# Kernel optimization log

Hardware: AMD Instinct MI355X
Metric: run time of the kernel (lower is better)

## Reference

```python
import jax, jax.numpy as jnp
import numpy as np

N_NODES = 100000
N_EDGES = 1600000
N_GRAPHS = 512
IN_DIM = 128
D = 128
N_CLASSES = 10


def gcn_layer(x, src, dst, W, b, n_nodes):
    """PyG GCNConv: out = D^{-1/2}(A+I)D^{-1/2} (x W) + b, deg over dst col + self-loop."""
    h = x @ W  # [N, d]
    deg = jax.ops.segment_sum(jnp.ones(src.shape[0], x.dtype), dst,
                              num_segments=n_nodes) + 1.0  # self-loop adds 1
    dinv = jax.lax.rsqrt(deg)  # deg >= 1 so always finite
    norm = dinv[src] * dinv[dst]  # [E]
    agg = jax.ops.segment_sum(h[src] * norm[:, None], dst, num_segments=n_nodes)
    agg = agg + h * (dinv * dinv)[:, None]  # self-loop message: dinv_i^2 * h_i
    return agg + b


def setup_inputs() -> dict:
    key = jax.random.key(0)
    ks = jax.random.split(key, 10)
    s = 0.05
    return {
        "x": jax.random.normal(ks[0], (N_NODES, IN_DIM), jnp.float32),
        "c_2": jax.random.randint(ks[1], (N_EDGES,), 0, N_NODES, jnp.int64),
        "u_2": jax.random.randint(ks[2], (N_EDGES,), 0, N_NODES, jnp.int64),
        "batch": jnp.sort(jax.random.randint(ks[3], (N_NODES,), 0, N_GRAPHS, jnp.int64)),
        "W_enc": jax.random.normal(ks[4], (IN_DIM, D), jnp.float32) * s,
        "b_enc": jnp.zeros((D,), jnp.float32),
        "W1": jax.random.normal(ks[5], (D, D), jnp.float32) * s,
        "b1": jnp.zeros((D,), jnp.float32),
        "W2": jax.random.normal(ks[6], (D, D), jnp.float32) * s,
        "b2": jnp.zeros((D,), jnp.float32),
        "W3": jax.random.normal(ks[7], (D, D), jnp.float32) * s,
        "b3": jnp.zeros((D,), jnp.float32),
        "Wr1": jax.random.normal(ks[8], (D, D), jnp.float32) * s,
        "br1": jnp.zeros((D,), jnp.float32),
        "Wr2": jax.random.normal(ks[9], (D, N_CLASSES), jnp.float32) * s,
        "br2": jnp.zeros((N_CLASSES,), jnp.float32),
    }


def reference(x, c_2, u_2, batch, W_enc, b_enc, W1, b1, W2, b2, W3, b3,
              Wr1, br1, Wr2, br2):
    h = x @ W_enc + b_enc
    for W, b in ((W1, b1), (W2, b2), (W3, b3)):
        h = gcn_layer(h, c_2, u_2, W, b, N_NODES)
        h = jax.nn.relu(h)  # dropout is identity in eval mode
    # global_add_pool over graph assignment
    g = jax.ops.segment_sum(h, batch, num_segments=N_GRAPHS)  # [G, d]
    logits = jax.nn.relu(g @ Wr1 + br1) @ Wr2 + br2  # [G, num_classes]
    return logits
```

## Files before the change

### kernel.cpp

```cpp
#include <hip/hip_runtime.h>
#include <hip/hip_bf16.h>

#define NN 100000
#define NE 1600000
#define NG 512
#define NC 10
#define NBINS 391
#define BINCAP 5120
#define EPB 4096

typedef __attribute__((ext_vector_type(8))) short bf16x8;
typedef __attribute__((ext_vector_type(4))) float f32x4;

__device__ __forceinline__ float bflo(unsigned u) { return __uint_as_float(u << 16); }
__device__ __forceinline__ float bfhi(unsigned u) { return __uint_as_float(u & 0xffff0000u); }
__device__ __forceinline__ unsigned short f2bf(float f) {
  unsigned u = __float_as_uint(f);
  unsigned r = u + 0x7fffu + ((u >> 16) & 1u);
  return (unsigned short)(r >> 16);
}


__global__ __launch_bounds__(256) void k_binp1(const int* __restrict__ src, const int* __restrict__ dst,
                                               int* __restrict__ binCursor, unsigned* __restrict__ stage) {
  __shared__ unsigned srec[EPB];
  __shared__ unsigned short sbin[EPB];
  __shared__ int cnt[NBINS], pre[NBINS], base[NBINS], lcur[NBINS];
  __shared__ int tmp[256];
  int t = threadIdx.x;
  for (int i = t; i < NBINS; i += 256) { cnt[i] = 0; lcur[i] = 0; }
  __syncthreads();
  int e0 = blockIdx.x * EPB;
  unsigned myrec[16];
  short mybin[16];
#pragma unroll
  for (int i = 0; i < 16; ++i) {
    int e = e0 + i * 256 + t;
    if (e < NE) {
      int s = src[e], d = dst[e];
      int b = d >> 8;
      mybin[i] = (short)b;
      myrec[i] = ((unsigned)s << 8) | (unsigned)(d & 255);
      atomicAdd(&cnt[b], 1);
    } else mybin[i] = -1;
  }
  __syncthreads();
  {
    int idx0 = t * 2;
    int c0 = (idx0 < NBINS) ? cnt[idx0] : 0;
    int c1 = (idx0 + 1 < NBINS) ? cnt[idx0 + 1] : 0;
    int s = c0 + c1;
    tmp[t] = s;
    __syncthreads();
    for (int o = 1; o < 256; o <<= 1) { int v = (t >= o) ? tmp[t - o] : 0; __syncthreads(); tmp[t] += v; __syncthreads(); }
    int ex = tmp[t] - s;
    if (idx0 < NBINS) pre[idx0] = ex;
    if (idx0 + 1 < NBINS) pre[idx0 + 1] = ex + c0;
  }
  __syncthreads();
  for (int i = t; i < NBINS; i += 256) if (cnt[i] > 0) base[i] = atomicAdd(&binCursor[i], cnt[i]);
  __syncthreads();
#pragma unroll
  for (int i = 0; i < 16; ++i) {
    int b = mybin[i];
    if (b >= 0) {
      int r = atomicAdd(&lcur[b], 1);
      int pos = pre[b] + r;
      srec[pos] = myrec[i];
      sbin[pos] = (unsigned short)b;
    }
  }
  __syncthreads();
  int total = NE - e0; if (total > EPB) total = EPB;
  for (int sidx = t; sidx < total; sidx += 256) {
    int b = sbin[sidx];
    stage[base[b] + (sidx - pre[b])] = srec[sidx];
  }
}

__global__ __launch_bounds__(256) void k_binp2(const unsigned* __restrict__ stage, const int* __restrict__ binCursor,
                                               int* __restrict__ csr_src, int* __restrict__ offs,
                                               int* __restrict__ deg, float* __restrict__ dinv) {
  __shared__ int ldeg[256], loff[256], lcur[256];
  __shared__ int tmp[256];
  int b = blockIdx.x, t = threadIdx.x;
  int n0 = b << 8;
  int sbase = b * BINCAP;
  int cnt = binCursor[b] - sbase; if (cnt > BINCAP) cnt = BINCAP;
  ldeg[t] = 0;
  lcur[t] = 0;
  __syncthreads();
  for (int j = t; j < cnt; j += 256) {
    unsigned r = stage[sbase + j];
    atomicAdd(&ldeg[r & 255], 1);
  }
  __syncthreads();
  int a = ldeg[t];
  tmp[t] = a;
  __syncthreads();
  for (int o = 1; o < 256; o <<= 1) { int v = (t >= o) ? tmp[t - o] : 0; __syncthreads(); tmp[t] += v; __syncthreads(); }
  int ex = tmp[t] - a;
  loff[t] = ex;
  int node = n0 + t;
  if (node < NN) {
    offs[node] = sbase + ex;
    deg[node] = a;
    dinv[node] = rsqrtf((float)a + 1.0f);
  }
  __syncthreads();
  for (int j = t; j < cnt; j += 256) {
    unsigned r = stage[sbase + j];
    int li = r & 255;
    int pos = atomicAdd(&lcur[li], 1);
    csr_src[sbase + loff[li] + pos] = (int)(r >> 8);
  }
}

__global__ __launch_bounds__(256) void k_wt4i(const float* __restrict__ Wa, const float* __restrict__ Wb,
                                              const float* __restrict__ Wc, const float* __restrict__ Wd,
                                              unsigned short* __restrict__ Ta, unsigned short* __restrict__ Tb,
                                              unsigned short* __restrict__ Tc, unsigned short* __restrict__ Td,
                                              int* __restrict__ binCursor) {
  if (blockIdx.x == 256) {
    for (int i = threadIdx.x; i < NBINS; i += 256) binCursor[i] = i * BINCAP;
    return;
  }
  int w = blockIdx.x >> 6;
  const float* W = (w == 0) ? Wa : (w == 1) ? Wb : (w == 2) ? Wc : Wd;
  unsigned short* T = (w == 0) ? Ta : (w == 1) ? Tb : (w == 2) ? Tc : Td;
  int idx = (blockIdx.x & 63) * 256 + threadIdx.x;
  int k = idx >> 7, c = idx & 127;
  T[c * 128 + k] = f2bf(W[k * 128 + c]);
}


template<int ADD_BIAS, int RELU, int SRC_F32, int SCALE_ROW>
__global__ __launch_bounds__(256) void k_gemm_mfma(const void* __restrict__ Ap,
                                                   const unsigned short* __restrict__ Wt,
                                                   const float* __restrict__ bias,
                                                   const float* __restrict__ dinv,
                                                   unsigned short* __restrict__ Out, int M) {
  __shared__ uint4 Al4[2048];
  __shared__ uint4 Wl4[2048];
  int row0 = blockIdx.x * 128;
  const uint4* W16 = (const uint4*)Wt;
  int lane = threadIdx.x & 63;
  int wid = threadIdx.x >> 6;

  if (!SRC_F32 && row0 + 128 <= M) {
    const uint4* A16 = (const uint4*)Ap;
    int rl = lane >> 4, cc = lane & 15;
#pragma unroll
    for (int it = 0; it < 8; ++it) {
      int rbase = it * 16 + wid * 4;
      int row = rbase + rl;
      int chunk = cc ^ (row & 15);
      __builtin_amdgcn_global_load_lds(
          (const __attribute__((address_space(1))) void*)(A16 + (size_t)(row0 + row) * 16 + chunk),
          (__attribute__((address_space(3))) void*)&Al4[rbase * 16], 16, 0, 0);
      __builtin_amdgcn_global_load_lds(
          (const __attribute__((address_space(1))) void*)(W16 + (size_t)row * 16 + chunk),
          (__attribute__((address_space(3))) void*)&Wl4[rbase * 16], 16, 0, 0);
    }
  } else {
#pragma unroll
    for (int it = 0; it < 8; ++it) {
      int idx = it * 256 + threadIdx.x;
      int r = idx >> 4, c = idx & 15;
      int gr = row0 + r;
      uint4 v = make_uint4(0, 0, 0, 0);
      if (gr < M) {
        if (SRC_F32) {
          const float4* Af = (const float4*)Ap;
          float4 f0 = Af[(size_t)gr * 32 + c * 2];
          float4 f1 = Af[(size_t)gr * 32 + c * 2 + 1];
          v.x = (unsigned)f2bf(f0.x) | ((unsigned)f2bf(f0.y) << 16);
          v.y = (unsigned)f2bf(f0.z) | ((unsigned)f2bf(f0.w) << 16);
          v.z = (unsigned)f2bf(f1.x) | ((unsigned)f2bf(f1.y) << 16);
          v.w = (unsigned)f2bf(f1.z) | ((unsigned)f2bf(f1.w) << 16);
        } else {
          v = ((const uint4*)Ap)[(size_t)gr * 16 + c];
        }
      }
      Al4[r * 16 + (c ^ (r & 15))] = v;
      Wl4[r * 16 + (c ^ (r & 15))] = W16[idx];
    }
  }
  __syncthreads();

  int wr = wid >> 1, wc = wid & 1;
  int lr = lane & 15, kb = lane >> 4;

  f32x4 acc[4][4] = {};
#pragma unroll
  for (int ks = 0; ks < 4; ++ks) {
    int c = ks * 4 + kb;
    bf16x8 af[4], bfr[4];
#pragma unroll
    for (int i = 0; i < 4; ++i) {
      int ar = wr * 64 + i * 16 + lr;
      af[i] = *(const bf16x8*)&Al4[ar * 16 + (c ^ lr)];
      int bc = wc * 64 + i * 16 + lr;
      bfr[i] = *(const bf16x8*)&Wl4[bc * 16 + (c ^ lr)];
    }
#pragma unroll
    for (int i = 0; i < 4; ++i)
#pragma unroll
      for (int n = 0; n < 4; ++n)
        acc[i][n] = __builtin_amdgcn_mfma_f32_16x16x32_bf16(af[i], bfr[n], acc[i][n], 0, 0, 0);
  }

  float bcol[4];
  if (ADD_BIAS) {
#pragma unroll
    for (int n = 0; n < 4; ++n) bcol[n] = bias[wc * 64 + n * 16 + lr];
  }
#pragma unroll
  for (int i = 0; i < 4; ++i) {
    int rbase = row0 + wr * 64 + i * 16 + kb * 4;
#pragma unroll
    for (int n = 0; n < 4; ++n) {
      int col = wc * 64 + n * 16 + lr;
#pragma unroll
      for (int j = 0; j < 4; ++j) {
        int gr = rbase + j;
        if (gr < M) {
          float v = acc[i][n][j];
          if (ADD_BIAS) v += bcol[n];
          if (RELU) v = fmaxf(v, 0.f);
          if (SCALE_ROW) v *= dinv[gr];
          Out[(size_t)gr * 128 + col] = f2bf(v);
        }
      }
    }
  }
}


__global__ __launch_bounds__(256) void k_agg(const unsigned short* __restrict__ hs,
                                             const int* __restrict__ offs, const int* __restrict__ deg,
                                             const float* __restrict__ dinv,
                                             const int* __restrict__ csr_src,
                                             const float* __restrict__ bias,
                                             unsigned short* __restrict__ out) {
  int node = blockIdx.x * 4 + (threadIdx.x >> 6);
  if (node >= NN) return;
  int l = threadIdx.x & 63;
  int q = l >> 4;
  int li = l & 15;
  const uint4* hs4 = (const uint4*)hs;
  float a0 = 0.f, a1 = 0.f, a2 = 0.f, a3 = 0.f, a4 = 0.f, a5 = 0.f, a6 = 0.f, a7 = 0.f;
  if (q == 0) {
    uint4 u = hs4[(size_t)node * 16 + li];
    a0 = bflo(u.x); a1 = bfhi(u.x); a2 = bflo(u.y); a3 = bfhi(u.y);
    a4 = bflo(u.z); a5 = bfhi(u.z); a6 = bflo(u.w); a7 = bfhi(u.w);
  }
  int p0 = offs[node], n = deg[node];
  int p = 0;
  for (; p + 16 <= n; p += 16) {
    int s0 = csr_src[p0 + p + q];
    int s1 = csr_src[p0 + p + 4 + q];
    int s2 = csr_src[p0 + p + 8 + q];
    int s3 = csr_src[p0 + p + 12 + q];
    uint4 u0 = hs4[(size_t)s0 * 16 + li];
    uint4 u1 = hs4[(size_t)s1 * 16 + li];
    uint4 u2 = hs4[(size_t)s2 * 16 + li];
    uint4 u3 = hs4[(size_t)s3 * 16 + li];
    a0 += bflo(u0.x) + bflo(u1.x) + bflo(u2.x) + bflo(u3.x);
    a1 += bfhi(u0.x) + bfhi(u1.x) + bfhi(u2.x) + bfhi(u3.x);
    a2 += bflo(u0.y) + bflo(u1.y) + bflo(u2.y) + bflo(u3.y);
    a3 += bfhi(u0.y) + bfhi(u1.y) + bfhi(u2.y) + bfhi(u3.y);
    a4 += bflo(u0.z) + bflo(u1.z) + bflo(u2.z) + bflo(u3.z);
    a5 += bfhi(u0.z) + bfhi(u1.z) + bfhi(u2.z) + bfhi(u3.z);
    a6 += bflo(u0.w) + bflo(u1.w) + bflo(u2.w) + bflo(u3.w);
    a7 += bfhi(u0.w) + bfhi(u1.w) + bfhi(u2.w) + bfhi(u3.w);
  }
  for (; p + 4 <= n; p += 4) {
    int s0 = csr_src[p0 + p + q];
    uint4 u = hs4[(size_t)s0 * 16 + li];
    a0 += bflo(u.x); a1 += bfhi(u.x); a2 += bflo(u.y); a3 += bfhi(u.y);
    a4 += bflo(u.z); a5 += bfhi(u.z); a6 += bflo(u.w); a7 += bfhi(u.w);
  }
  int rem = n - p;
  if (q < rem) {
    int s0 = csr_src[p0 + p + q];
    uint4 u = hs4[(size_t)s0 * 16 + li];
    a0 += bflo(u.x); a1 += bfhi(u.x); a2 += bflo(u.y); a3 += bfhi(u.y);
    a4 += bflo(u.z); a5 += bfhi(u.z); a6 += bflo(u.w); a7 += bfhi(u.w);
  }
  a0 += __shfl_xor(a0, 16); a0 += __shfl_xor(a0, 32);
  a1 += __shfl_xor(a1, 16); a1 += __shfl_xor(a1, 32);
  a2 += __shfl_xor(a2, 16); a2 += __shfl_xor(a2, 32);
  a3 += __shfl_xor(a3, 16); a3 += __shfl_xor(a3, 32);
  a4 += __shfl_xor(a4, 16); a4 += __shfl_xor(a4, 32);
  a5 += __shfl_xor(a5, 16); a5 += __shfl_xor(a5, 32);
  a6 += __shfl_xor(a6, 16); a6 += __shfl_xor(a6, 32);
  a7 += __shfl_xor(a7, 16); a7 += __shfl_xor(a7, 32);
  if (q == 0) {
    float di = dinv[node];
    float4 b0 = ((const float4*)bias)[li * 2];
    float4 b1 = ((const float4*)bias)[li * 2 + 1];
    float r0 = fmaxf(fmaf(a0, di, b0.x), 0.f);
    float r1 = fmaxf(fmaf(a1, di, b0.y), 0.f);
    float r2 = fmaxf(fmaf(a2, di, b0.z), 0.f);
    float r3 = fmaxf(fmaf(a3, di, b0.w), 0.f);
    float r4 = fmaxf(fmaf(a4, di, b1.x), 0.f);
    float r5 = fmaxf(fmaf(a5, di, b1.y), 0.f);
    float r6 = fmaxf(fmaf(a6, di, b1.z), 0.f);
    float r7 = fmaxf(fmaf(a7, di, b1.w), 0.f);
    uint4 o;
    o.x = (unsigned)f2bf(r0) | ((unsigned)f2bf(r1) << 16);
    o.y = (unsigned)f2bf(r2) | ((unsigned)f2bf(r3) << 16);
    o.z = (unsigned)f2bf(r4) | ((unsigned)f2bf(r5) << 16);
    o.w = (unsigned)f2bf(r6) | ((unsigned)f2bf(r7) << 16);
    ((uint4*)out)[(size_t)node * 16 + li] = o;
  }
}


__device__ __forceinline__ int lowerb(const int* a, int n, int key) {
  int lo = 0, hi = n;
  while (lo < hi) {
    int mid = (lo + hi) >> 1;
    if (a[mid] < key) lo = mid + 1; else hi = mid;
  }
  return lo;
}

__global__ __launch_bounds__(256) void k_pool(const unsigned short* __restrict__ h, const int* __restrict__ batch,
                                              float* __restrict__ g) {
  __shared__ float sx[4][64];
  __shared__ float sy[4][64];
  int gi = blockIdx.x;
  int col = threadIdx.x & 63;
  int rp = threadIdx.x >> 6;
  int lo = lowerb(batch, NN, gi), hi = lowerb(batch, NN, gi + 1);
  const unsigned* h32 = (const unsigned*)h;
  float ax = 0.f, ay = 0.f;
  for (int i = lo + rp; i < hi; i += 4) {
    unsigned u = h32[(size_t)i * 64 + col];
    ax += bflo(u);
    ay += bfhi(u);
  }
  sx[rp][col] = ax;
  sy[rp][col] = ay;
  __syncthreads();
  if (rp == 0) {
    ax = sx[0][col] + sx[1][col] + sx[2][col] + sx[3][col];
    ay = sy[0][col] + sy[1][col] + sy[2][col] + sy[3][col];
    ((float2*)g)[gi * 64 + col] = make_float2(ax, ay);
  }
}

__global__ __launch_bounds__(256) void k_gemm_f32(const float* __restrict__ A, const float* __restrict__ W,
                                                  const float* __restrict__ bias, float* __restrict__ Out,
                                                  int M) {
  __shared__ float4 Wl[128 * 32];
  __shared__ float4 Xl[128 * 32];
  const float4* W4 = (const float4*)W;
  for (int i = threadIdx.x; i < 4096; i += 256) Wl[i] = W4[i];
  int row0 = blockIdx.x * 128;
  const float4* A4 = (const float4*)A;
  for (int i = threadIdx.x; i < 4096; i += 256) {
    int r = i >> 5, g = i & 31;
    int gr = row0 + r;
    float4 v = make_float4(0.f, 0.f, 0.f, 0.f);
    if (gr < M) v = A4[gr * 32 + g];
    Xl[r * 32 + (g ^ ((r >> 3) & 7))] = v;
  }
  __syncthreads();

  int cg = threadIdx.x & 15;
  int rg = threadIdx.x >> 4;
  int swz = rg & 7;
  float acc[8][8] = {};
  for (int g = 0; g < 32; ++g) {
    float4 xv[8];
#pragma unroll
    for (int i = 0; i < 8; ++i) xv[i] = Xl[(rg * 8 + i) * 32 + (g ^ swz)];
#pragma unroll
    for (int kk = 0; kk < 4; ++kk) {
      float4 wa = Wl[(g * 4 + kk) * 32 + cg * 2];
      float4 wb = Wl[(g * 4 + kk) * 32 + cg * 2 + 1];
#pragma unroll
      for (int i = 0; i < 8; ++i) {
        float x = (kk == 0) ? xv[i].x : (kk == 1) ? xv[i].y : (kk == 2) ? xv[i].z : xv[i].w;
        acc[i][0] = fmaf(x, wa.x, acc[i][0]);
        acc[i][1] = fmaf(x, wa.y, acc[i][1]);
        acc[i][2] = fmaf(x, wa.z, acc[i][2]);
        acc[i][3] = fmaf(x, wa.w, acc[i][3]);
        acc[i][4] = fmaf(x, wb.x, acc[i][4]);
        acc[i][5] = fmaf(x, wb.y, acc[i][5]);
        acc[i][6] = fmaf(x, wb.z, acc[i][6]);
        acc[i][7] = fmaf(x, wb.w, acc[i][7]);
      }
    }
  }
  float4 ba = ((const float4*)bias)[cg * 2];
  float4 bb = ((const float4*)bias)[cg * 2 + 1];
#pragma unroll
  for (int i = 0; i < 8; ++i) {
    int gr = row0 + rg * 8 + i;
    if (gr < M) {
      float4 oa, ob;
      oa.x = fmaxf(acc[i][0] + ba.x, 0.f); oa.y = fmaxf(acc[i][1] + ba.y, 0.f);
      oa.z = fmaxf(acc[i][2] + ba.z, 0.f); oa.w = fmaxf(acc[i][3] + ba.w, 0.f);
      ob.x = fmaxf(acc[i][4] + bb.x, 0.f); ob.y = fmaxf(acc[i][5] + bb.y, 0.f);
      ob.z = fmaxf(acc[i][6] + bb.z, 0.f); ob.w = fmaxf(acc[i][7] + bb.w, 0.f);
      ((float4*)Out)[gr * 32 + cg * 2] = oa;
      ((float4*)Out)[gr * 32 + cg * 2 + 1] = ob;
    }
  }
}

__global__ __launch_bounds__(128) void k_cls(const float* __restrict__ t, const float* __restrict__ Wr2,
                                             const float* __restrict__ br2, float* __restrict__ out) {
  int gi = blockIdx.x;
  __shared__ float row[128];
  row[threadIdx.x] = t[gi * 128 + threadIdx.x];
  __syncthreads();
  if (threadIdx.x < NC) {
    float acc = br2[threadIdx.x];
    for (int k = 0; k < 128; ++k) acc = fmaf(row[k], Wr2[k * NC + threadIdx.x], acc);
    out[gi * NC + threadIdx.x] = acc;
  }
}


extern "C" void kernel_launch(void* const* d_in, const int* in_sizes, int n_in,
                              void* d_out, int out_size, void* d_ws, size_t ws_size,
                              hipStream_t stream) {
  const float* x     = (const float*)d_in[0];
  const int*   src   = (const int*)d_in[1];
  const int*   dst   = (const int*)d_in[2];
  const int*   batch = (const int*)d_in[3];
  const float* W_enc = (const float*)d_in[4];
  const float* b_enc = (const float*)d_in[5];
  const float* W1 = (const float*)d_in[6],  *b1 = (const float*)d_in[7];
  const float* W2 = (const float*)d_in[8],  *b2 = (const float*)d_in[9];
  const float* W3 = (const float*)d_in[10], *b3 = (const float*)d_in[11];
  const float* Wr1 = (const float*)d_in[12], *br1 = (const float*)d_in[13];
  const float* Wr2 = (const float*)d_in[14], *br2 = (const float*)d_in[15];
  float* out = (float*)d_out;

  char* ws = (char*)d_ws;
  size_t off = 0;
  auto alloc = [&](size_t bytes) {
    void* p = ws + off;
    off = (off + bytes + 255) & ~(size_t)255;
    return p;
  };
  unsigned short* h   = (unsigned short*)alloc((size_t)NN * 128 * 2);
  unsigned short* hs  = (unsigned short*)alloc((size_t)NN * 128 * 2);
  unsigned short* WtE = (unsigned short*)alloc(128 * 128 * 2);
  unsigned short* Wt1 = (unsigned short*)alloc(128 * 128 * 2);
  unsigned short* Wt2 = (unsigned short*)alloc(128 * 128 * 2);
  unsigned short* Wt3 = (unsigned short*)alloc(128 * 128 * 2);
  int*   deg      = (int*)alloc((size_t)NN * 4);
  float* dinv     = (float*)alloc((size_t)NN * 4);
  int*   offs     = (int*)alloc((size_t)NN * 4);
  int*   binCursor= (int*)alloc(NBINS * 4);
  int*   csr_src  = (int*)alloc((size_t)NBINS * BINCAP * 4);
  unsigned* stage = (unsigned*)alloc((size_t)NBINS * BINCAP * 4);
  float* g        = (float*)alloc((size_t)NG * 128 * 4);
  float* t1       = (float*)alloc((size_t)NG * 128 * 4);

  k_wt4i<<<257, 256, 0, stream>>>(W_enc, W1, W2, W3, WtE, Wt1, Wt2, Wt3, binCursor);
  k_binp1<<<(NE + EPB - 1) / EPB, 256, 0, stream>>>(src, dst, binCursor, stage);
  k_binp2<<<NBINS, 256, 0, stream>>>(stage, binCursor, csr_src, offs, deg, dinv);

  int gM = (NN + 127) / 128;
  k_gemm_mfma<1, 0, 1, 0><<<gM, 256, 0, stream>>>(x, WtE, b_enc, nullptr, h, NN);

  const unsigned short* Wts[3] = {Wt1, Wt2, Wt3};
  const float* bs[3] = {b1, b2, b3};
  int gA = (NN + 3) / 4;
  for (int L = 0; L < 3; ++L) {
    k_gemm_mfma<0, 0, 0, 1><<<gM, 256, 0, stream>>>(h, Wts[L], nullptr, dinv, hs, NN);
    k_agg<<<gA, 256, 0, stream>>>(hs, offs, deg, dinv, csr_src, bs[L], h);
  }

  k_pool<<<NG, 256, 0, stream>>>(h, batch, g);
  k_gemm_f32<<<(NG + 127) / 128, 256, 0, stream>>>(g, Wr1, br1, t1, NG);
  k_cls<<<NG, 128, 0, stream>>>(t1, Wr2, br2, out);
}
```

Measured before the change: 399.9 us.

## Store GEMM output in feature-sliced layout and aggregate per slice

```diff
diff --git a/kernel.cpp b/kernel.cpp
--- a/kernel.cpp
+++ b/kernel.cpp
@@ -8,6 +8,7 @@
 #define NBINS 391
 #define BINCAP 5120
 #define EPB 4096
+#define NSL 8
 
 typedef __attribute__((ext_vector_type(8))) short bf16x8;
 typedef __attribute__((ext_vector_type(4))) float f32x4;
@@ -134,7 +135,7 @@
 }
 
 
-template<int ADD_BIAS, int RELU, int SRC_F32, int SCALE_ROW>
+template<int ADD_BIAS, int RELU, int SRC_F32, int SCALE_ROW, int STORE_SLICED>
 __global__ __launch_bounds__(256) void k_gemm_mfma(const void* __restrict__ Ap,
                                                    const unsigned short* __restrict__ Wt,
                                                    const float* __restrict__ bias,
@@ -229,7 +230,10 @@
           if (ADD_BIAS) v += bcol[n];
           if (RELU) v = fmaxf(v, 0.f);
           if (SCALE_ROW) v *= dinv[gr];
-          Out[(size_t)gr * 128 + col] = f2bf(v);
+          if (STORE_SLICED)
+            Out[((size_t)(col >> 4) * NN + gr) * 16 + (col & 15)] = f2bf(v);
+          else
+            Out[(size_t)gr * 128 + col] = f2bf(v);
         }
       }
     }
@@ -237,83 +241,41 @@
 }
 
 
-__global__ __launch_bounds__(256) void k_agg(const unsigned short* __restrict__ hs,
+__global__ __launch_bounds__(256) void k_agg(const unsigned short* __restrict__ hs_s,
                                              const int* __restrict__ offs, const int* __restrict__ deg,
                                              const float* __restrict__ dinv,
                                              const int* __restrict__ csr_src,
                                              const float* __restrict__ bias,
                                              unsigned short* __restrict__ out) {
-  int node = blockIdx.x * 4 + (threadIdx.x >> 6);
-  if (node >= NN) return;
-  int l = threadIdx.x & 63;
-  int q = l >> 4;
-  int li = l & 15;
-  const uint4* hs4 = (const uint4*)hs;
-  float a0 = 0.f, a1 = 0.f, a2 = 0.f, a3 = 0.f, a4 = 0.f, a5 = 0.f, a6 = 0.f, a7 = 0.f;
-  if (q == 0) {
-    uint4 u = hs4[(size_t)node * 16 + li];
-    a0 = bflo(u.x); a1 = bfhi(u.x); a2 = bflo(u.y); a3 = bfhi(u.y);
-    a4 = bflo(u.z); a5 = bfhi(u.z); a6 = bflo(u.w); a7 = bfhi(u.w);
-  }
-  int p0 = offs[node], n = deg[node];
-  int p = 0;
-  for (; p + 16 <= n; p += 16) {
-    int s0 = csr_src[p0 + p + q];
-    int s1 = csr_src[p0 + p + 4 + q];
-    int s2 = csr_src[p0 + p + 8 + q];
-    int s3 = csr_src[p0 + p + 12 + q];
-    uint4 u0 = hs4[(size_t)s0 * 16 + li];
-    uint4 u1 = hs4[(size_t)s1 * 16 + li];
-    uint4 u2 = hs4[(size_t)s2 * 16 + li];
-    uint4 u3 = hs4[(size_t)s3 * 16 + li];
-    a0 += bflo(u0.x) + bflo(u1.x) + bflo(u2.x) + bflo(u3.x);
-    a1 += bfhi(u0.x) + bfhi(u1.x) + bfhi(u2.x) + bfhi(u3.x);
-    a2 += bflo(u0.y) + bflo(u1.y) + bflo(u2.y) + bflo(u3.y);
-    a3 += bfhi(u0.y) + bfhi(u1.y) + bfhi(u2.y) + bfhi(u3.y);
-    a4 += bflo(u0.z) + bflo(u1.z) + bflo(u2.z) + bflo(u3.z);
-    a5 += bfhi(u0.z) + bfhi(u1.z) + bfhi(u2.z) + bfhi(u3.z);
-    a6 += bflo(u0.w) + bflo(u1.w) + bflo(u2.w) + bflo(u3.w);
-    a7 += bfhi(u0.w) + bfhi(u1.w) + bfhi(u2.w) + bfhi(u3.w);
-  }
-  for (; p + 4 <= n; p += 4) {
-    int s0 = csr_src[p0 + p + q];
-    uint4 u = hs4[(size_t)s0 * 16 + li];
-    a0 += bflo(u.x); a1 += bfhi(u.x); a2 += bflo(u.y); a3 += bfhi(u.y);
-    a4 += bflo(u.z); a5 += bfhi(u.z); a6 += bflo(u.w); a7 += bfhi(u.w);
-  }
-  int rem = n - p;
-  if (q < rem) {
-    int s0 = csr_src[p0 + p + q];
-    uint4 u = hs4[(size_t)s0 * 16 + li];
-    a0 += bflo(u.x); a1 += bfhi(u.x); a2 += bflo(u.y); a3 += bfhi(u.y);
-    a4 += bflo(u.z); a5 += bfhi(u.z); a6 += bflo(u.w); a7 += bfhi(u.w);
-  }
-  a0 += __shfl_xor(a0, 16); a0 += __shfl_xor(a0, 32);
-  a1 += __shfl_xor(a1, 16); a1 += __shfl_xor(a1, 32);
-  a2 += __shfl_xor(a2, 16); a2 += __shfl_xor(a2, 32);
-  a3 += __shfl_xor(a3, 16); a3 += __shfl_xor(a3, 32);
-  a4 += __shfl_xor(a4, 16); a4 += __shfl_xor(a4, 32);
-  a5 += __shfl_xor(a5, 16); a5 += __shfl_xor(a5, 32);
-  a6 += __shfl_xor(a6, 16); a6 += __shfl_xor(a6, 32);
-  a7 += __shfl_xor(a7, 16); a7 += __shfl_xor(a7, 32);
-  if (q == 0) {
-    float di = dinv[node];
-    float4 b0 = ((const float4*)bias)[li * 2];
-    float4 b1 = ((const float4*)bias)[li * 2 + 1];
-    float r0 = fmaxf(fmaf(a0, di, b0.x), 0.f);
-    float r1 = fmaxf(fmaf(a1, di, b0.y), 0.f);
-    float r2 = fmaxf(fmaf(a2, di, b0.z), 0.f);
-    float r3 = fmaxf(fmaf(a3, di, b0.w), 0.f);
-    float r4 = fmaxf(fmaf(a4, di, b1.x), 0.f);
-    float r5 = fmaxf(fmaf(a5, di, b1.y), 0.f);
-    float r6 = fmaxf(fmaf(a6, di, b1.z), 0.f);
-    float r7 = fmaxf(fmaf(a7, di, b1.w), 0.f);
-    uint4 o;
-    o.x = (unsigned)f2bf(r0) | ((unsigned)f2bf(r1) << 16);
-    o.y = (unsigned)f2bf(r2) | ((unsigned)f2bf(r3) << 16);
-    o.z = (unsigned)f2bf(r4) | ((unsigned)f2bf(r5) << 16);
-    o.w = (unsigned)f2bf(r6) | ((unsigned)f2bf(r7) << 16);
-    ((uint4*)out)[(size_t)node * 16 + li] = o;
+  int s = blockIdx.x & 7;
+  int g = blockIdx.x >> 3;
+  int wv = threadIdx.x >> 6, lane = threadIdx.x & 63;
+  int q = lane >> 3, li = lane & 7;
+  const unsigned* base = (const unsigned*)hs_s + (size_t)s * NN * 8;
+#pragma unroll
+  for (int i = 0; i < 8; ++i) {
+    int node = g * 32 + wv * 8 + i;
+    if (node >= NN) return;
+    int p0 = __builtin_nontemporal_load(&offs[node]);
+    int n  = __builtin_nontemporal_load(&deg[node]);
+    unsigned su = base[(size_t)node * 8 + li];
+    float a0 = (q == 0) ? bflo(su) : 0.f;
+    float a1 = (q == 0) ? bfhi(su) : 0.f;
+    for (int p = q; p < n; p += 8) {
+      int sidx = __builtin_nontemporal_load(&csr_src[p0 + p]);
+      unsigned u = base[(size_t)sidx * 8 + li];
+      a0 += bflo(u);
+      a1 += bfhi(u);
+    }
+    a0 += __shfl_xor(a0, 8); a0 += __shfl_xor(a0, 16); a0 += __shfl_xor(a0, 32);
+    a1 += __shfl_xor(a1, 8); a1 += __shfl_xor(a1, 16); a1 += __shfl_xor(a1, 32);
+    if (q == 0) {
+      float di = dinv[node];
+      float2 b2 = ((const float2*)bias)[s * 8 + li];
+      float r0 = fmaxf(fmaf(a0, di, b2.x), 0.f);
+      float r1 = fmaxf(fmaf(a1, di, b2.y), 0.f);
+      ((unsigned*)out)[(size_t)node * 64 + s * 8 + li] = (unsigned)f2bf(r0) | ((unsigned)f2bf(r1) << 16);
+    }
   }
 }
 
@@ -470,13 +432,13 @@
   k_binp2<<<NBINS, 256, 0, stream>>>(stage, binCursor, csr_src, offs, deg, dinv);
 
   int gM = (NN + 127) / 128;
-  k_gemm_mfma<1, 0, 1, 0><<<gM, 256, 0, stream>>>(x, WtE, b_enc, nullptr, h, NN);
+  k_gemm_mfma<1, 0, 1, 0, 0><<<gM, 256, 0, stream>>>(x, WtE, b_enc, nullptr, h, NN);
 
   const unsigned short* Wts[3] = {Wt1, Wt2, Wt3};
   const float* bs[3] = {b1, b2, b3};
-  int gA = (NN + 3) / 4;
+  int gA = ((NN + 31) / 32) * NSL;
   for (int L = 0; L < 3; ++L) {
-    k_gemm_mfma<0, 0, 0, 1><<<gM, 256, 0, stream>>>(h, Wts[L], nullptr, dinv, hs, NN);
+    k_gemm_mfma<0, 0, 0, 1, 1><<<gM, 256, 0, stream>>>(h, Wts[L], nullptr, dinv, hs, NN);
     k_agg<<<gA, 256, 0, stream>>>(hs, offs, deg, dinv, csr_src, bs[L], h);
   }
 
```

Measured after the change: 1.303 ms. 3.26x slower.
